# Kernel tuning notes

Measured on AMD Instinct MI355X. Metric: run time of the kernel, lower is better.

Reference implementation:

```python
import jax, jax.numpy as jnp
import numpy as np

D_MODEL = 192
DEPTH = 16
D_INNER = 384   # expand=2
D_STATE = 16
D_CONV = 4
DT_RANK = 12    # ceil(192/16)
J = 42
T = 8
NUM_CLASSES = 1000
B = 64
EPS = 1e-5


def setup_inputs() -> dict:
    key = jax.random.key(0)
    ks = jax.random.split(key, 16)

    def n(k, shape, scale=0.02):
        return jax.random.normal(k, shape, jnp.float32) * scale

    dt_bias_init = float(np.log(np.expm1(0.01)))  # softplus^-1(0.01), mamba dt init
    A_init = jnp.log(jnp.tile(jnp.arange(1, D_STATE + 1, dtype=jnp.float32), (DEPTH, D_INNER, 1)))
    return {
        "x": jax.random.normal(ks[0], (B, T, J, 3), jnp.float32),
        "joint_embed_w": n(ks[1], (D_MODEL, 3)),
        "joint_embed_b": jnp.zeros((D_MODEL,), jnp.float32),
        "cls_token": n(ks[2], (1, 1, D_MODEL)),
        "spatial_pos": n(ks[3], (1, J + 1, D_MODEL)),
        "temporal_pos": n(ks[4], (1, T, D_MODEL)),
        "norm_w": jnp.ones((DEPTH, D_MODEL), jnp.float32),
        "in_proj_w": n(ks[5], (DEPTH, 2 * D_INNER, D_MODEL)),
        "conv_w": n(ks[6], (DEPTH, D_INNER, D_CONV), 0.1),
        "conv_b": jnp.zeros((DEPTH, D_INNER), jnp.float32),
        "x_proj_w": n(ks[7], (DEPTH, DT_RANK + 2 * D_STATE, D_INNER)),
        "dt_proj_w": n(ks[8], (DEPTH, D_INNER, DT_RANK), DT_RANK ** -0.5),
        "dt_proj_b": jnp.full((DEPTH, D_INNER), dt_bias_init, jnp.float32),
        "A_log": A_init,
        "Dp": jnp.ones((DEPTH, D_INNER), jnp.float32),
        "out_proj_w": n(ks[9], (DEPTH, D_MODEL, D_INNER)),
        "norm_f_w": jnp.ones((D_MODEL,), jnp.float32),
        "head_w": n(ks[10], (NUM_CLASSES, D_MODEL)),
        "head_b": jnp.zeros((NUM_CLASSES,), jnp.float32),
    }


def rmsnorm(x, w):
    return x * jax.lax.rsqrt(jnp.mean(x * x, axis=-1, keepdims=True) + EPS) * w


def mamba(x, in_w, cw, cb, xp_w, dtw, dtb, A_log, Dp, ow):
    # x: (B, L, d_model)
    Bsz, L, _ = x.shape
    xz = jnp.einsum('bld,ed->ble', x, in_w)          # (B,L,2*di)
    u, z = jnp.split(xz, 2, axis=-1)
    # depthwise causal conv over time
    uc = jnp.transpose(u, (0, 2, 1))                  # (B,di,L)
    uc = jnp.pad(uc, ((0, 0), (0, 0), (D_CONV - 1, 0)))
    uc = jax.lax.conv_general_dilated(
        uc, cw[:, None, :], (1,), 'VALID',
        dimension_numbers=('NCH', 'OIH', 'NCH'),
        feature_group_count=D_INNER) + cb[None, :, None]
    u = jax.nn.silu(jnp.transpose(uc, (0, 2, 1)))     # (B,L,di)
    dbl = jnp.einsum('bld,ed->ble', u, xp_w)          # (B,L,dt_rank+2*ds)
    dt, Bm, Cm = jnp.split(dbl, [DT_RANK, DT_RANK + D_STATE], axis=-1)
    delta = jax.nn.softplus(jnp.einsum('blr,dr->bld', dt, dtw) + dtb)  # (B,L,di)
    A = -jnp.exp(A_log)                               # (di,ds)

    def step(h, xs):
        d_t, B_t, C_t, u_t = xs                       # (B,di),(B,ds),(B,ds),(B,di)
        h = h * jnp.exp(d_t[..., None] * A) + (d_t * u_t)[..., None] * B_t[:, None, :]
        return h, jnp.einsum('bds,bs->bd', h, C_t)

    xs = (jnp.swapaxes(delta, 0, 1), jnp.swapaxes(Bm, 0, 1),
          jnp.swapaxes(Cm, 0, 1), jnp.swapaxes(u, 0, 1))
    h0 = jnp.zeros((Bsz, D_INNER, D_STATE), x.dtype)
    _, ys = jax.lax.scan(step, h0, xs)                # (L,B,di)
    y = jnp.swapaxes(ys, 0, 1) + u * Dp
    y = y * jax.nn.silu(z)
    return jnp.einsum('ble,de->bld', y, ow)


def reference(x, joint_embed_w, joint_embed_b, cls_token, spatial_pos, temporal_pos,
              norm_w, in_proj_w, conv_w, conv_b, x_proj_w, dt_proj_w, dt_proj_b,
              A_log, Dp, out_proj_w, norm_f_w, head_w, head_b):
    Bq, Tq, Jq, _ = x.shape
    xe = jnp.einsum('btjc,dc->btjd', x, joint_embed_w) + joint_embed_b
    xe = xe.reshape(Bq * Tq, Jq, D_MODEL)
    cls = jnp.broadcast_to(cls_token, (Bq * Tq, 1, D_MODEL))
    xcat = jnp.concatenate([cls, xe], axis=1) + spatial_pos   # (B*T, J+1, M)
    cls_tokens = xcat[:Bq, :1, :]
    body = xcat[:, 1:, :].reshape(Bq, Tq, Jq, D_MODEL)
    body = body.transpose(0, 2, 1, 3).reshape(Bq * Jq, Tq, D_MODEL) + temporal_pos
    body = body.reshape(Bq, Jq, Tq, D_MODEL).transpose(0, 2, 1, 3).reshape(Bq, Tq * Jq, D_MODEL)
    h = jnp.concatenate([cls_tokens, body], axis=1)           # (B, 1+T*J, M)

    residual = None
    for i in range(DEPTH):
        residual = h + residual if residual is not None else h
        hn = rmsnorm(residual, norm_w[i])
        h = mamba(hn, in_proj_w[i], conv_w[i], conv_b[i], x_proj_w[i],
                  dt_proj_w[i], dt_proj_b[i], A_log[i], Dp[i], out_proj_w[i])
    residual = h + residual
    feat = rmsnorm(residual, norm_f_w)[:, 0, :]
    return feat @ head_w.T + head_b
```

## Files before the change

kernel.cpp:

```cpp
#include <hip/hip_runtime.h>
#include <hip/hip_bf16.h>
#include <math.h>

#define B_ 64
#define T_ 8
#define J_ 42
#define L_ 337
#define D_ 192
#define E_ 384
#define S_ 16
#define R_ 12
#define DEPTH_ 16
#define NC_ 1000
#define M_ (B_*L_)
#define XZW_ (2*E_)
#define DBLW_ (R_+2*S_)
#define EPS_ 1e-5f
#define CH_ 16
#define NCH_ 22
#define EG_ (E_/8)
#define LOG2E_ 1.44269504088896f

typedef float    f32x4  __attribute__((ext_vector_type(4)));
typedef unsigned u32x4  __attribute__((ext_vector_type(4)));
typedef __bf16   bf16x8 __attribute__((ext_vector_type(8)));
typedef unsigned short ushort8 __attribute__((ext_vector_type(8)));

__device__ __forceinline__ float sigmoid_(float x){ return 1.f/(1.f+__expf(-x)); }
__device__ __forceinline__ float softplus_(float x){
  return (x > 20.f) ? x : __logf(1.f + __expf(x));
}
__device__ __forceinline__ unsigned short f2bf(float f){
  unsigned u = __float_as_uint(f);
  unsigned r = (u + 0x7fffu + ((u>>16)&1u)) >> 16;
  return (unsigned short)r;
}
__device__ __forceinline__ float bf2f(unsigned short h){
  return __uint_as_float(((unsigned)h)<<16);
}

__global__ void cvt_bf16_kernel(const float* __restrict__ in,
                                unsigned short* __restrict__ out, int n){
  int i = blockIdx.x*blockDim.x + threadIdx.x;
  if (i < n) out[i] = f2bf(in[i]);
}

__global__ void scan_prep_kernel(const float* __restrict__ dtw,
                                 const float* __restrict__ A_log,
                                 float* __restrict__ dtwT,
                                 float* __restrict__ a1v){
  int idx = blockIdx.x*blockDim.x + threadIdx.x;
  if (idx >= DEPTH_*E_) return;
  int d = idx % E_;
  int i = idx / E_;
  a1v[idx] = -__expf(A_log[((size_t)i*E_ + d)*S_]) * LOG2E_;
  #pragma unroll
  for (int r=0;r<R_;r++)
    dtwT[((size_t)i*R_ + r)*E_ + d] = dtw[((size_t)i*E_ + d)*R_ + r];
}

__global__ void embed_kernel(const float* __restrict__ x,
                             const float* __restrict__ jw,
                             const float* __restrict__ jb,
                             const float* __restrict__ cls,
                             const float* __restrict__ sp,
                             const float* __restrict__ tp,
                             float* __restrict__ res) {
  int idx = blockIdx.x*blockDim.x + threadIdx.x;
  if (idx >= M_*D_) return;
  int d = idx % D_;
  int m = idx / D_;
  int l = m % L_;
  int b = m / L_;
  float v;
  if (l == 0) {
    v = cls[d] + sp[d];
  } else {
    int lm = l-1, t = lm / J_, j = lm % J_;
    const float* xp = x + ((size_t)((b*T_+t)*J_ + j))*3;
    v = jb[d] + sp[(1+j)*D_+d] + tp[t*D_+d]
      + xp[0]*jw[d*3+0] + xp[1]*jw[d*3+1] + xp[2]*jw[d*3+2];
  }
  res[idx] = v;
}

__global__ __launch_bounds__(64) void norm0_kernel(const float* __restrict__ residual,
    const float* __restrict__ w, unsigned short* __restrict__ hn) {
  int m = blockIdx.x;
  int lane = threadIdx.x;
  size_t base = (size_t)m*D_;
  float r[3];
  float ss = 0.f;
  #pragma unroll
  for (int i=0;i<3;i++){
    int d = lane + i*64;
    r[i] = residual[base+d];
    ss += r[i]*r[i];
  }
  #pragma unroll
  for (int off=32; off>=1; off>>=1) ss += __shfl_xor(ss, off, 64);
  float sc = rsqrtf(ss*(1.f/(float)D_) + EPS_);
  #pragma unroll
  for (int i=0;i<3;i++){
    int d = lane + i*64;
    hn[base+d] = f2bf(r[i]*sc*w[d]);
  }
}

__global__ __launch_bounds__(256) void gemm_in(
    const unsigned short* __restrict__ A,
    const unsigned short* __restrict__ W,
    unsigned short* __restrict__ u_raw,
    unsigned short* __restrict__ z)
{
  const int wave = threadIdx.x >> 6;
  const int lane = threadIdx.x & 63;
  const int row0 = blockIdx.x * 64;
  const int col0 = (blockIdx.y * 4 + wave) * 64;
  const int lr = lane & 15;
  const int lk = (lane >> 4) * 8;
  f32x4 acc[4][4] = {};
  for (int k0 = 0; k0 < D_; k0 += 32) {
    bf16x8 af[4], bfr[4];
    #pragma unroll
    for (int i=0;i<4;i++)
      af[i] = __builtin_bit_cast(bf16x8,
          *(const u32x4*)(A + (size_t)(row0 + i*16 + lr)*D_ + k0 + lk));
    #pragma unroll
    for (int j=0;j<4;j++)
      bfr[j] = __builtin_bit_cast(bf16x8,
          *(const u32x4*)(W + (size_t)(col0 + j*16 + lr)*D_ + k0 + lk));
    #pragma unroll
    for (int i=0;i<4;i++)
      #pragma unroll
      for (int j=0;j<4;j++)
        acc[i][j] = __builtin_amdgcn_mfma_f32_16x16x32_bf16(af[i], bfr[j], acc[i][j], 0, 0, 0);
  }
  const int ro = (lane >> 4) * 4;
  unsigned short* dst = (col0 < E_) ? u_raw : z;
  const int cbase = (col0 < E_) ? col0 : (col0 - E_);
  #pragma unroll
  for (int i=0;i<4;i++)
    #pragma unroll
    for (int j=0;j<4;j++){
      int col = cbase + j*16 + lr;
      #pragma unroll
      for (int r=0;r<4;r++){
        int row = row0 + i*16 + ro + r;
        dst[(size_t)row*E_ + col] = f2bf(acc[i][j][r]);
      }
    }
}

__global__ __launch_bounds__(256) void gemm_xp(
    const unsigned short* __restrict__ A,
    const unsigned short* __restrict__ W,
    float* __restrict__ C)
{
  const int wave = threadIdx.x >> 6;
  const int lane = threadIdx.x & 63;
  const int row0 = blockIdx.x * 64 + wave * 16;
  const int lr = lane & 15;
  const int lk = (lane >> 4) * 8;
  const bf16x8 bzero = __builtin_bit_cast(bf16x8, (u32x4)(0u));
  f32x4 acc[3] = {};
  for (int k0 = 0; k0 < E_; k0 += 32) {
    bf16x8 af = __builtin_bit_cast(bf16x8,
        *(const u32x4*)(A + (size_t)(row0 + lr)*E_ + k0 + lk));
    #pragma unroll
    for (int j=0;j<3;j++){
      int col = j*16 + lr;
      bf16x8 bfr = (col < DBLW_) ? __builtin_bit_cast(bf16x8,
          *(const u32x4*)(W + (size_t)col*E_ + k0 + lk)) : bzero;
      acc[j] = __builtin_amdgcn_mfma_f32_16x16x32_bf16(af, bfr, acc[j], 0, 0, 0);
    }
  }
  const int ro = (lane >> 4) * 4;
  #pragma unroll
  for (int j=0;j<3;j++){
    int col = j*16 + lr;
    if (col >= DBLW_) continue;
    #pragma unroll
    for (int r=0;r<4;r++){
      int row = row0 + ro + r;
      C[(size_t)row*DBLW_ + col] = acc[j][r];
    }
  }
}

__global__ __launch_bounds__(256) void conv_silu_kernel(
    const unsigned short* __restrict__ u_raw,
    const float* __restrict__ cw,
    const float* __restrict__ cb,
    unsigned short* __restrict__ u2) {
  int idx = blockIdx.x*blockDim.x + threadIdx.x;
  if (idx >= M_*EG_) return;
  const int g = idx % EG_;
  const int m = idx / EG_;
  const int l = m % L_;
  const int d0 = g*8;
  float4 wr[8];
  #pragma unroll
  for (int j=0;j<8;j++) wr[j] = *(const float4*)(cw + (size_t)(d0+j)*4);
  float acc[8];
  {
    float4 b0 = *(const float4*)(cb + d0);
    float4 b1 = *(const float4*)(cb + d0 + 4);
    acc[0]=b0.x; acc[1]=b0.y; acc[2]=b0.z; acc[3]=b0.w;
    acc[4]=b1.x; acc[5]=b1.y; acc[6]=b1.z; acc[7]=b1.w;
  }
  #pragma unroll
  for (int k=0;k<4;k++){
    const int lk = l + k - 3;
    if (lk < 0) continue;
    const ushort8 v = *(const ushort8*)(u_raw + (size_t)(m + k - 3)*E_ + d0);
    #pragma unroll
    for (int j=0;j<8;j++){
      float tap = (k==0)?wr[j].x:(k==1)?wr[j].y:(k==2)?wr[j].z:wr[j].w;
      acc[j] = fmaf(tap, bf2f(v[j]), acc[j]);
    }
  }
  ushort8 o;
  #pragma unroll
  for (int j=0;j<8;j++){
    float a = acc[j];
    o[j] = f2bf(a * sigmoid_(a));
  }
  *(ushort8*)(u2 + (size_t)m*E_ + d0) = o;
}

__global__ __launch_bounds__(128) void scan_partA(
    const float* __restrict__ dbl,
    const unsigned short* __restrict__ u2,
    const float* __restrict__ dtwT,
    const float* __restrict__ dtb,
    const float* __restrict__ a1v,
    unsigned short* __restrict__ part_h,
    float* __restrict__ part_sd)
{
  const int b = blockIdx.x;
  const int d = blockIdx.y*128 + threadIdx.x;
  const int c = blockIdx.z;
  float dtw_r[R_];
  #pragma unroll
  for (int r=0;r<R_;r++) dtw_r[r] = dtwT[r*E_+d];
  const float dtb_r = dtb[d];
  const float a1 = a1v[d];
  float h[S_];
  #pragma unroll
  for (int s=0;s<S_;s++) h[s] = 0.f;
  float sum_dl = 0.f;
  const size_t m0 = (size_t)b*L_ + (size_t)c*CH_;

  for (int t=0; t<CH_; ++t) {
    const float4* dr = (const float4*)(dbl + (m0+t)*DBLW_);
    float4 q0=dr[0],q1=dr[1],q2=dr[2],q3=dr[3],q4=dr[4],q5=dr[5],q6=dr[6];
    const float u_ = bf2f(u2[(m0+t)*E_ + d]);
    float s0 = fmaf(q0.y,dtw_r[1], q0.x*dtw_r[0]);
    s0 = fmaf(q0.z,dtw_r[2], s0); s0 = fmaf(q0.w,dtw_r[3], s0);
    float s1 = fmaf(q1.y,dtw_r[5], q1.x*dtw_r[4]);
    s1 = fmaf(q1.z,dtw_r[6], s1); s1 = fmaf(q1.w,dtw_r[7], s1);
    float s2 = fmaf(q2.y,dtw_r[9], fmaf(q2.x,dtw_r[8], dtb_r));
    s2 = fmaf(q2.z,dtw_r[10], s2); s2 = fmaf(q2.w,dtw_r[11], s2);
    float dtv = softplus_((s0+s1)+s2);
    sum_dl += dtv;
    const float du = dtv * u_;
    const float rr = exp2f(dtv * a1);
    const float rr2 = rr*rr, rr3 = rr2*rr, rr4 = rr2*rr2;
    float p0=rr, p1=rr2, p2=rr3, p3=rr4;
    h[0]=fmaf(h[0],p0,du*q3.x); h[1]=fmaf(h[1],p1,du*q3.y);
    h[2]=fmaf(h[2],p2,du*q3.z); h[3]=fmaf(h[3],p3,du*q3.w);
    p0*=rr4; p1*=rr4; p2*=rr4; p3*=rr4;
    h[4]=fmaf(h[4],p0,du*q4.x); h[5]=fmaf(h[5],p1,du*q4.y);
    h[6]=fmaf(h[6],p2,du*q4.z); h[7]=fmaf(h[7],p3,du*q4.w);
    p0*=rr4; p1*=rr4; p2*=rr4; p3*=rr4;
    h[8]=fmaf(h[8],p0,du*q5.x);  h[9]=fmaf(h[9],p1,du*q5.y);
    h[10]=fmaf(h[10],p2,du*q5.z); h[11]=fmaf(h[11],p3,du*q5.w);
    p0*=rr4; p1*=rr4; p2*=rr4; p3*=rr4;
    h[12]=fmaf(h[12],p0,du*q6.x); h[13]=fmaf(h[13],p1,du*q6.y);
    h[14]=fmaf(h[14],p2,du*q6.z); h[15]=fmaf(h[15],p3,du*q6.w);
  }
  const size_t pb = (size_t)b*NCH_ + c;
  #pragma unroll
  for (int s=0;s<S_;s++) part_h[(pb*S_ + s)*E_ + d] = f2bf(h[s]);
  part_sd[pb*E_ + d] = sum_dl;
}

__global__ __launch_bounds__(256) void scan_combine(
    unsigned short* __restrict__ part_h,
    const float* __restrict__ part_sd,
    const float* __restrict__ a1v)
{
  int idx = blockIdx.x*blockDim.x + threadIdx.x;
  const int d = idx % E_;
  const int s = (idx / E_) % S_;
  const int b = idx / (E_*S_);
  const float a1s = a1v[d] * (float)(s+1);
  float hprev = 0.f;
  for (int c=0; c<NCH_-1; ++c) {
    const size_t off = (((size_t)b*NCH_ + c)*S_ + s)*E_ + d;
    const float tmp = bf2f(part_h[off]);
    part_h[off] = f2bf(hprev);
    const float sd = part_sd[((size_t)b*NCH_ + c)*E_ + d];
    hprev = fmaf(hprev, exp2f(a1s*sd), tmp);
  }
  part_h[(((size_t)b*NCH_ + NCH_-1)*S_ + s)*E_ + d] = f2bf(hprev);
}

__global__ __launch_bounds__(128) void scan_partC(
    const float* __restrict__ dbl,
    const unsigned short* __restrict__ u2,
    const unsigned short* __restrict__ zbuf,
    const float* __restrict__ dtwT, const float* __restrict__ dtb,
    const float* __restrict__ a1v, const float* __restrict__ Dp,
    const unsigned short* __restrict__ part_h,
    unsigned short* __restrict__ y)
{
  const int b = blockIdx.x;
  const int d = blockIdx.y*128 + threadIdx.x;
  const int c = blockIdx.z;
  const int t0 = c*CH_;
  const int nt = (t0 + CH_ <= L_) ? CH_ : (L_ - t0);
  float dtw_r[R_];
  #pragma unroll
  for (int r=0;r<R_;r++) dtw_r[r] = dtwT[r*E_+d];
  const float dtb_r = dtb[d];
  const float dpv   = Dp[d];
  const float a1 = a1v[d];
  float h[S_];
  {
    const size_t pb = (size_t)b*NCH_ + c;
    #pragma unroll
    for (int s=0;s<S_;s++) h[s] = bf2f(part_h[(pb*S_ + s)*E_ + d]);
  }
  const size_t m0 = (size_t)b*L_ + t0;

  for (int t=0; t<nt; ++t) {
    const float4* dr = (const float4*)(dbl + (m0+t)*DBLW_);
    float4 q0=dr[0],q1=dr[1],q2=dr[2],q3=dr[3],q4=dr[4],q5=dr[5],
           q6=dr[6],q7=dr[7],q8=dr[8],q9=dr[9],q10=dr[10];
    const float u_ = bf2f(u2[(m0+t)*E_ + d]);
    const float z_ = bf2f(zbuf[(m0+t)*E_ + d]);
    float s0 = fmaf(q0.y,dtw_r[1], q0.x*dtw_r[0]);
    s0 = fmaf(q0.z,dtw_r[2], s0); s0 = fmaf(q0.w,dtw_r[3], s0);
    float s1 = fmaf(q1.y,dtw_r[5], q1.x*dtw_r[4]);
    s1 = fmaf(q1.z,dtw_r[6], s1); s1 = fmaf(q1.w,dtw_r[7], s1);
    float s2 = fmaf(q2.y,dtw_r[9], fmaf(q2.x,dtw_r[8], dtb_r));
    s2 = fmaf(q2.z,dtw_r[10], s2); s2 = fmaf(q2.w,dtw_r[11], s2);
    float dtv = softplus_((s0+s1)+s2);
    const float du = dtv * u_;
    const float rr = exp2f(dtv * a1);
    const float rr2 = rr*rr, rr3 = rr2*rr, rr4 = rr2*rr2;
    float p0=rr, p1=rr2, p2=rr3, p3=rr4;
    float a0,a1_,a2,a3;
    h[0]=fmaf(h[0],p0,du*q3.x); a0=h[0]*q7.x;
    h[1]=fmaf(h[1],p1,du*q3.y); a1_=h[1]*q7.y;
    h[2]=fmaf(h[2],p2,du*q3.z); a2=h[2]*q7.z;
    h[3]=fmaf(h[3],p3,du*q3.w); a3=h[3]*q7.w;
    p0*=rr4; p1*=rr4; p2*=rr4; p3*=rr4;
    h[4]=fmaf(h[4],p0,du*q4.x); a0=fmaf(h[4],q8.x,a0);
    h[5]=fmaf(h[5],p1,du*q4.y); a1_=fmaf(h[5],q8.y,a1_);
    h[6]=fmaf(h[6],p2,du*q4.z); a2=fmaf(h[6],q8.z,a2);
    h[7]=fmaf(h[7],p3,du*q4.w); a3=fmaf(h[7],q8.w,a3);
    p0*=rr4; p1*=rr4; p2*=rr4; p3*=rr4;
    h[8]=fmaf(h[8],p0,du*q5.x);  a0=fmaf(h[8],q9.x,a0);
    h[9]=fmaf(h[9],p1,du*q5.y);  a1_=fmaf(h[9],q9.y,a1_);
    h[10]=fmaf(h[10],p2,du*q5.z); a2=fmaf(h[10],q9.z,a2);
    h[11]=fmaf(h[11],p3,du*q5.w); a3=fmaf(h[11],q9.w,a3);
    p0*=rr4; p1*=rr4; p2*=rr4; p3*=rr4;
    h[12]=fmaf(h[12],p0,du*q6.x); a0=fmaf(h[12],q10.x,a0);
    h[13]=fmaf(h[13],p1,du*q6.y); a1_=fmaf(h[13],q10.y,a1_);
    h[14]=fmaf(h[14],p2,du*q6.z); a2=fmaf(h[14],q10.z,a2);
    h[15]=fmaf(h[15],p3,du*q6.w); a3=fmaf(h[15],q10.w,a3);
    const float accv = (a0+a1_)+(a2+a3);
    const float yv = fmaf(u_, dpv, accv) * (z_ * sigmoid_(z_));
    y[(m0+t)*E_ + d] = f2bf(yv);
  }
}

__global__ __launch_bounds__(768) void gemm_out_fused(
    const unsigned short* __restrict__ A,
    const unsigned short* __restrict__ W,
    float* __restrict__ residual,
    const float* __restrict__ wnext,
    unsigned short* __restrict__ hn)
{
  const int wave = threadIdx.x >> 6;
  const int lane = threadIdx.x & 63;
  const int roww = wave & 3;
  const int colw = wave >> 2;
  const int row0 = blockIdx.x * 64 + roww * 16;
  const int col0 = colw * 64;
  const int lr = lane & 15;
  const int lk = (lane >> 4) * 8;
  f32x4 acc[4] = {};
  for (int k0 = 0; k0 < E_; k0 += 32) {
    bf16x8 af = __builtin_bit_cast(bf16x8,
        *(const u32x4*)(A + (size_t)(row0 + lr)*E_ + k0 + lk));
    #pragma unroll
    for (int j=0;j<4;j++){
      bf16x8 bfr = __builtin_bit_cast(bf16x8,
          *(const u32x4*)(W + (size_t)(col0 + j*16 + lr)*E_ + k0 + lk));
      acc[j] = __builtin_amdgcn_mfma_f32_16x16x32_bf16(af, bfr, acc[j], 0, 0, 0);
    }
  }
  const int ro = (lane >> 4) * 4;
  __shared__ float rs[3][64];
  float wn[4];
  #pragma unroll
  for (int j=0;j<4;j++) wn[j] = wnext[col0 + j*16 + lr];
  #pragma unroll
  for (int r=0;r<4;r++){
    int row = row0 + ro + r;
    float psum = 0.f;
    #pragma unroll
    for (int j=0;j<4;j++){
      int col = col0 + j*16 + lr;
      float v = residual[(size_t)row*D_ + col] + acc[j][r];
      acc[j][r] = v;
      residual[(size_t)row*D_ + col] = v;
      psum = fmaf(v, v, psum);
    }
    psum += __shfl_xor(psum, 1);
    psum += __shfl_xor(psum, 2);
    psum += __shfl_xor(psum, 4);
    psum += __shfl_xor(psum, 8);
    if (lr == 0) rs[colw][roww*16 + ro + r] = psum;
  }
  __syncthreads();
  #pragma unroll
  for (int r=0;r<4;r++){
    int rloc = roww*16 + ro + r;
    float tot = rs[0][rloc] + rs[1][rloc] + rs[2][rloc];
    float sc = rsqrtf(tot*(1.f/(float)D_) + EPS_);
    int row = row0 + ro + r;
    #pragma unroll
    for (int j=0;j<4;j++){
      int col = col0 + j*16 + lr;
      hn[(size_t)row*D_ + col] = f2bf(acc[j][r]*sc*wn[j]);
    }
  }
}

__global__ __launch_bounds__(256) void final_head_kernel(
    const float* __restrict__ residual, const float* __restrict__ w,
    const float* __restrict__ hw, const float* __restrict__ hb,
    float* __restrict__ out) {
  __shared__ float fs[D_];
  __shared__ float red[4];
  const int b = blockIdx.x;
  const int tid = threadIdx.x;
  const size_t base = (size_t)b*L_*D_;
  float v = (tid < D_) ? residual[base+tid] : 0.f;
  float ss = v*v;
  #pragma unroll
  for (int off=32; off>=1; off>>=1) ss += __shfl_xor(ss, off, 64);
  if ((tid & 63) == 0) red[tid>>6] = ss;
  __syncthreads();
  const float tot = red[0]+red[1]+red[2]+red[3];
  const float sc = rsqrtf(tot*(1.f/(float)D_) + EPS_);
  if (tid < D_) fs[tid] = v*sc*w[tid];
  __syncthreads();
  for (int n=tid;n<NC_;n+=256){
    float acc = hb[n];
    #pragma unroll 4
    for (int k=0;k<D_;k++) acc += fs[k]*hw[(size_t)n*D_+k];
    out[(size_t)b*NC_+n] = acc;
  }
}

extern "C" void kernel_launch(void* const* d_in, const int* in_sizes, int n_in,
                              void* d_out, int out_size, void* d_ws, size_t ws_size,
                              hipStream_t stream) {
  const float* x        = (const float*)d_in[0];
  const float* jw       = (const float*)d_in[1];
  const float* jb       = (const float*)d_in[2];
  const float* cls      = (const float*)d_in[3];
  const float* sp       = (const float*)d_in[4];
  const float* tp       = (const float*)d_in[5];
  const float* norm_w   = (const float*)d_in[6];
  const float* in_w     = (const float*)d_in[7];
  const float* conv_w   = (const float*)d_in[8];
  const float* conv_b   = (const float*)d_in[9];
  const float* xp_w     = (const float*)d_in[10];
  const float* dt_w     = (const float*)d_in[11];
  const float* dt_b     = (const float*)d_in[12];
  const float* A_log    = (const float*)d_in[13];
  const float* Dp       = (const float*)d_in[14];
  const float* out_w    = (const float*)d_in[15];
  const float* norm_f_w = (const float*)d_in[16];
  const float* head_w   = (const float*)d_in[17];
  const float* head_b   = (const float*)d_in[18];
  float* out = (float*)d_out;

  float* ws = (float*)d_ws;
  float* residual = ws;
  float* dbl      = residual + (size_t)M_*D_;
  float* part_sd  = dbl      + (size_t)M_*DBLW_;
  float* dtwT     = part_sd  + (size_t)B_*NCH_*E_;
  float* a1v      = dtwT     + (size_t)DEPTH_*R_*E_;
  unsigned short* bw = (unsigned short*)(a1v + (size_t)DEPTH_*E_);
  unsigned short* hn     = bw;
  unsigned short* u_raw  = hn     + (size_t)M_*D_;
  unsigned short* zbuf   = u_raw  + (size_t)M_*E_;
  unsigned short* u2     = zbuf   + (size_t)M_*E_;
  unsigned short* ybuf   = u2     + (size_t)M_*E_;
  unsigned short* part_h = ybuf   + (size_t)M_*E_;
  unsigned short* w_in   = part_h + (size_t)B_*NCH_*S_*E_;
  unsigned short* w_xp   = w_in   + (size_t)DEPTH_*XZW_*D_;
  unsigned short* w_out  = w_xp   + (size_t)DEPTH_*DBLW_*E_;

  {
    int n1 = DEPTH_*XZW_*D_;
    int n2 = DEPTH_*DBLW_*E_;
    int n3 = DEPTH_*D_*E_;
    cvt_bf16_kernel<<<(n1+255)/256, 256, 0, stream>>>(in_w,  w_in,  n1);
    cvt_bf16_kernel<<<(n2+255)/256, 256, 0, stream>>>(xp_w,  w_xp,  n2);
    cvt_bf16_kernel<<<(n3+255)/256, 256, 0, stream>>>(out_w, w_out, n3);
    scan_prep_kernel<<<(DEPTH_*E_+255)/256, 256, 0, stream>>>(dt_w, A_log, dtwT, a1v);
  }

  embed_kernel<<<(M_*D_+255)/256, 256, 0, stream>>>(x, jw, jb, cls, sp, tp, residual);
  norm0_kernel<<<M_, 64, 0, stream>>>(residual, norm_w, hn);

  for (int i = 0; i < DEPTH_; ++i) {
    gemm_in<<<dim3(M_/64, XZW_/256), 256, 0, stream>>>(
        hn, w_in + (size_t)i*XZW_*D_, u_raw, zbuf);
    conv_silu_kernel<<<(M_*EG_+255)/256, 256, 0, stream>>>(
        u_raw, conv_w + (size_t)i*E_*4, conv_b + (size_t)i*E_, u2);
    gemm_xp<<<M_/64, 256, 0, stream>>>(
        u2, w_xp + (size_t)i*DBLW_*E_, dbl);
    scan_partA<<<dim3(B_, E_/128, NCH_-1), 128, 0, stream>>>(
        dbl, u2, dtwT + (size_t)i*R_*E_, dt_b + (size_t)i*E_,
        a1v + (size_t)i*E_, part_h, part_sd);
    scan_combine<<<(B_*S_*E_)/256, 256, 0, stream>>>(
        part_h, part_sd, a1v + (size_t)i*E_);
    scan_partC<<<dim3(B_, E_/128, NCH_), 128, 0, stream>>>(
        dbl, u2, zbuf, dtwT + (size_t)i*R_*E_, dt_b + (size_t)i*E_,
        a1v + (size_t)i*E_, Dp + (size_t)i*E_, part_h, ybuf);
    const float* wnext = (i+1 < DEPTH_) ? (norm_w + (size_t)(i+1)*D_) : norm_f_w;
    gemm_out_fused<<<M_/64, 768, 0, stream>>>(
        ybuf, w_out + (size_t)i*D_*E_, residual, wnext, hn);
  }

  final_head_kernel<<<B_, 256, 0, stream>>>(residual, norm_f_w, head_w, head_b, out);
}
```

Measured before the change: 2.953 ms.

## Fuse embedding with first RMSNorm and retile out-projection GEMM to 4x4 per wave

The embedding and initial RMSNorm now run in one kernel with one block per row, so the residual is not written and then read back. The out-projection GEMM with its fused residual-add and norm drops from 12 waves (each a 16x64 tile) to 3 waves, each computing a 64x64 tile from 4 A and 4 B fragments. Each loaded fragment now feeds four MFMAs instead of one. The cost is more accumulator registers per wave and fewer waves per block, which may reduce latency hiding and occupancy.

```diff
diff --git a/kernel.cpp b/kernel.cpp
--- a/kernel.cpp
+++ b/kernel.cpp
@@ -59,50 +59,48 @@
     dtwT[((size_t)i*R_ + r)*E_ + d] = dtw[((size_t)i*E_ + d)*R_ + r];
 }
 
-__global__ void embed_kernel(const float* __restrict__ x,
-                             const float* __restrict__ jw,
-                             const float* __restrict__ jb,
-                             const float* __restrict__ cls,
-                             const float* __restrict__ sp,
-                             const float* __restrict__ tp,
-                             float* __restrict__ res) {
-  int idx = blockIdx.x*blockDim.x + threadIdx.x;
-  if (idx >= M_*D_) return;
-  int d = idx % D_;
-  int m = idx / D_;
-  int l = m % L_;
-  int b = m / L_;
-  float v;
+__global__ __launch_bounds__(64) void embed_norm0_kernel(
+    const float* __restrict__ x,
+    const float* __restrict__ jw,
+    const float* __restrict__ jb,
+    const float* __restrict__ cls,
+    const float* __restrict__ sp,
+    const float* __restrict__ tp,
+    const float* __restrict__ w,
+    float* __restrict__ res,
+    unsigned short* __restrict__ hn) {
+  const int m = blockIdx.x;
+  const int lane = threadIdx.x;
+  const int l = m % L_;
+  const size_t base = (size_t)m*D_;
+  float r[3]; float ss = 0.f;
   if (l == 0) {
-    v = cls[d] + sp[d];
+    #pragma unroll
+    for (int i=0;i<3;i++){
+      int d = lane + i*64;
+      r[i] = cls[d] + sp[d];
+      ss += r[i]*r[i];
+    }
   } else {
-    int lm = l-1, t = lm / J_, j = lm % J_;
+    const int lm = l-1, t = lm / J_, j = lm % J_;
+    const int b = m / L_;
     const float* xp = x + ((size_t)((b*T_+t)*J_ + j))*3;
-    v = jb[d] + sp[(1+j)*D_+d] + tp[t*D_+d]
-      + xp[0]*jw[d*3+0] + xp[1]*jw[d*3+1] + xp[2]*jw[d*3+2];
-  }
-  res[idx] = v;
-}
-
-__global__ __launch_bounds__(64) void norm0_kernel(const float* __restrict__ residual,
-    const float* __restrict__ w, unsigned short* __restrict__ hn) {
-  int m = blockIdx.x;
-  int lane = threadIdx.x;
-  size_t base = (size_t)m*D_;
-  float r[3];
-  float ss = 0.f;
+    const float x0 = xp[0], x1 = xp[1], x2 = xp[2];
+    #pragma unroll
+    for (int i=0;i<3;i++){
+      int d = lane + i*64;
+      r[i] = jb[d] + sp[(1+j)*D_+d] + tp[t*D_+d]
+           + x0*jw[d*3+0] + x1*jw[d*3+1] + x2*jw[d*3+2];
+      ss += r[i]*r[i];
+    }
+  }
+  #pragma unroll
+  for (int off=32; off>=1; off>>=1) ss += __shfl_xor(ss, off, 64);
+  float sc = rsqrtf(ss*(1.f/(float)D_) + EPS_);
   #pragma unroll
   for (int i=0;i<3;i++){
     int d = lane + i*64;
-    r[i] = residual[base+d];
-    ss += r[i]*r[i];
-  }
-  #pragma unroll
-  for (int off=32; off>=1; off>>=1) ss += __shfl_xor(ss, off, 64);
-  float sc = rsqrtf(ss*(1.f/(float)D_) + EPS_);
-  #pragma unroll
-  for (int i=0;i<3;i++){
-    int d = lane + i*64;
+    res[base+d] = r[i];
     hn[base+d] = f2bf(r[i]*sc*w[d]);
   }
 }
@@ -378,7 +376,7 @@
   }
 }
 
-__global__ __launch_bounds__(768) void gemm_out_fused(
+__global__ __launch_bounds__(192) void gemm_out_fused(
     const unsigned short* __restrict__ A,
     const unsigned short* __restrict__ W,
     float* __restrict__ residual,
@@ -387,22 +385,26 @@
 {
   const int wave = threadIdx.x >> 6;
   const int lane = threadIdx.x & 63;
-  const int roww = wave & 3;
-  const int colw = wave >> 2;
-  const int row0 = blockIdx.x * 64 + roww * 16;
-  const int col0 = colw * 64;
+  const int row0 = blockIdx.x * 64;
+  const int col0 = wave * 64;
   const int lr = lane & 15;
   const int lk = (lane >> 4) * 8;
-  f32x4 acc[4] = {};
+  f32x4 acc[4][4] = {};
   for (int k0 = 0; k0 < E_; k0 += 32) {
-    bf16x8 af = __builtin_bit_cast(bf16x8,
-        *(const u32x4*)(A + (size_t)(row0 + lr)*E_ + k0 + lk));
-    #pragma unroll
-    for (int j=0;j<4;j++){
-      bf16x8 bfr = __builtin_bit_cast(bf16x8,
+    bf16x8 af[4], bfr[4];
+    #pragma unroll
+    for (int i=0;i<4;i++)
+      af[i] = __builtin_bit_cast(bf16x8,
+          *(const u32x4*)(A + (size_t)(row0 + i*16 + lr)*E_ + k0 + lk));
+    #pragma unroll
+    for (int j=0;j<4;j++)
+      bfr[j] = __builtin_bit_cast(bf16x8,
           *(const u32x4*)(W + (size_t)(col0 + j*16 + lr)*E_ + k0 + lk));
-      acc[j] = __builtin_amdgcn_mfma_f32_16x16x32_bf16(af, bfr, acc[j], 0, 0, 0);
-    }
+    #pragma unroll
+    for (int i=0;i<4;i++)
+      #pragma unroll
+      for (int j=0;j<4;j++)
+        acc[i][j] = __builtin_amdgcn_mfma_f32_16x16x32_bf16(af[i], bfr[j], acc[i][j], 0, 0, 0);
   }
   const int ro = (lane >> 4) * 4;
   __shared__ float rs[3][64];
@@ -410,34 +412,40 @@
   #pragma unroll
   for (int j=0;j<4;j++) wn[j] = wnext[col0 + j*16 + lr];
   #pragma unroll
-  for (int r=0;r<4;r++){
-    int row = row0 + ro + r;
-    float psum = 0.f;
-    #pragma unroll
-    for (int j=0;j<4;j++){
-      int col = col0 + j*16 + lr;
-      float v = residual[(size_t)row*D_ + col] + acc[j][r];
-      acc[j][r] = v;
-      residual[(size_t)row*D_ + col] = v;
-      psum = fmaf(v, v, psum);
-    }
-    psum += __shfl_xor(psum, 1);
-    psum += __shfl_xor(psum, 2);
-    psum += __shfl_xor(psum, 4);
-    psum += __shfl_xor(psum, 8);
-    if (lr == 0) rs[colw][roww*16 + ro + r] = psum;
+  for (int i=0;i<4;i++){
+    #pragma unroll
+    for (int r=0;r<4;r++){
+      int row = row0 + i*16 + ro + r;
+      float psum = 0.f;
+      #pragma unroll
+      for (int j=0;j<4;j++){
+        int col = col0 + j*16 + lr;
+        float v = residual[(size_t)row*D_ + col] + acc[i][j][r];
+        acc[i][j][r] = v;
+        residual[(size_t)row*D_ + col] = v;
+        psum = fmaf(v, v, psum);
+      }
+      psum += __shfl_xor(psum, 1);
+      psum += __shfl_xor(psum, 2);
+      psum += __shfl_xor(psum, 4);
+      psum += __shfl_xor(psum, 8);
+      if (lr == 0) rs[wave][i*16 + ro + r] = psum;
+    }
   }
   __syncthreads();
   #pragma unroll
-  for (int r=0;r<4;r++){
-    int rloc = roww*16 + ro + r;
-    float tot = rs[0][rloc] + rs[1][rloc] + rs[2][rloc];
-    float sc = rsqrtf(tot*(1.f/(float)D_) + EPS_);
-    int row = row0 + ro + r;
-    #pragma unroll
-    for (int j=0;j<4;j++){
-      int col = col0 + j*16 + lr;
-      hn[(size_t)row*D_ + col] = f2bf(acc[j][r]*sc*wn[j]);
+  for (int i=0;i<4;i++){
+    #pragma unroll
+    for (int r=0;r<4;r++){
+      int rloc = i*16 + ro + r;
+      float tot = rs[0][rloc] + rs[1][rloc] + rs[2][rloc];
+      float sc = rsqrtf(tot*(1.f/(float)D_) + EPS_);
+      int row = row0 + rloc;
+      #pragma unroll
+      for (int j=0;j<4;j++){
+        int col = col0 + j*16 + lr;
+        hn[(size_t)row*D_ + col] = f2bf(acc[i][j][r]*sc*wn[j]);
+      }
     }
   }
 }
@@ -520,8 +528,8 @@
     scan_prep_kernel<<<(DEPTH_*E_+255)/256, 256, 0, stream>>>(dt_w, A_log, dtwT, a1v);
   }
 
-  embed_kernel<<<(M_*D_+255)/256, 256, 0, stream>>>(x, jw, jb, cls, sp, tp, residual);
-  norm0_kernel<<<M_, 64, 0, stream>>>(residual, norm_w, hn);
+  embed_norm0_kernel<<<M_, 64, 0, stream>>>(x, jw, jb, cls, sp, tp, norm_w,
+                                            residual, hn);
 
   for (int i = 0; i < DEPTH_; ++i) {
     gemm_in<<<dim3(M_/64, XZW_/256), 256, 0, stream>>>(
@@ -539,7 +547,7 @@
         dbl, u2, zbuf, dtwT + (size_t)i*R_*E_, dt_b + (size_t)i*E_,
         a1v + (size_t)i*E_, Dp + (size_t)i*E_, part_h, ybuf);
     const float* wnext = (i+1 < DEPTH_) ? (norm_w + (size_t)(i+1)*D_) : norm_f_w;
-    gemm_out_fused<<<M_/64, 768, 0, stream>>>(
+    gemm_out_fused<<<M_/64, 192, 0, stream>>>(
         ybuf, w_out + (size_t)i*D_*E_, residual, wnext, hn);
   }
 
```

After: 2.711 ms. 1.09x faster.
